# Kernel optimization log

Hardware: AMD Instinct MI355X
Metric: run time of the kernel (lower is better)

The kernel has to match this reference:

```python
import jax, jax.numpy as jnp
import numpy as np

HIDDEN = 1024
HEADS = 16
HEAD_DIM = HIDDEN // HEADS
B, S = 2, 2048


def setup_inputs() -> dict:
    key = jax.random.key(0)
    k1, k2, k3 = jax.random.split(key, 3)
    scale_in = 1.0 / np.sqrt(HIDDEN)
    x = jax.random.normal(k1, (B, S, HIDDEN), dtype=jnp.float32)
    wqkv_w = jax.random.normal(k2, (3 * HIDDEN, HIDDEN), dtype=jnp.float32) * scale_in
    wo_w = jax.random.normal(k3, (HIDDEN, HIDDEN), dtype=jnp.float32) * scale_in
    wo_b = jnp.zeros((HIDDEN,), dtype=jnp.float32)
    return {"x": x, "wqkv_w": wqkv_w, "wo_w": wo_w, "wo_b": wo_b}


def reference(x, wqkv_w, wo_w, wo_b):
    b, s, d = x.shape
    h, hd = HEADS, HEAD_DIM
    sm_scale = hd ** (-0.5)
    # QKV projection (torch Linear: x @ W^T), then chunk into q,k,v
    qkv = jnp.einsum('bsd,ed->bse', x, wqkv_w)  # [b, s, 3d]
    q, k, v = jnp.split(qkv, 3, axis=-1)
    # [b, h, s, hd]
    q = q.reshape(b, s, h, hd).transpose(0, 2, 1, 3)
    k = k.reshape(b, s, h, hd).transpose(0, 2, 1, 3)
    v = v.reshape(b, s, h, hd).transpose(0, 2, 1, 3)
    # raw scores, then causal mask (mask applied BEFORE scaling, as in source;
    # -inf * scale == -inf so math matches softmax(score*scale) with mask)
    scores = jnp.einsum('bhqe,bhke->bhqk', q, k)
    causal = jnp.tril(jnp.ones((s, s), dtype=bool))
    scores = jnp.where(causal[None, None, :, :], scores, -jnp.inf)
    weights = jax.nn.softmax(scores * sm_scale, axis=-1)
    # dropout p=0.0 (eval) -> identity
    out = jnp.einsum('bhqk,bhke->bhqe', weights, v)
    out = out.transpose(0, 2, 1, 3).reshape(b, s, h * hd)
    y = jnp.einsum('bsd,ed->bse', out, wo_w) + wo_b
    return (y, k, v)
```

## Files before the change

kernel.cpp:

```cpp
#include <hip/hip_runtime.h>
#include <cstdint>
#include <cstddef>


using bf16x8 = __attribute__((ext_vector_type(8))) __bf16;
using f32x4  = __attribute__((ext_vector_type(4))) float;
using u16    = unsigned short;

#define SOFT_SCALE 0.1803368801111244f

__device__ __forceinline__ u16 f2bf(float f) {
  union { float f; uint32_t u; } a; a.f = f;
  uint32_t r = a.u + 0x7fffu + ((a.u >> 16) & 1u);
  return (u16)(r >> 16);
}

__device__ __forceinline__ bf16x8 ldfrag(const u16* p) {
  return *reinterpret_cast<const bf16x8*>(p);
}

__device__ __forceinline__ void gload_lds16(const void* g, void* l) {
  __builtin_amdgcn_global_load_lds((const __attribute__((address_space(1))) void*)g,
                                   (__attribute__((address_space(3))) void*)l,
                                   16, 0, 0);
}

__device__ __forceinline__ uint32_t cvt_pk_bf16(float a, float b) {
  uint32_t r;
  asm("v_cvt_pk_bf16_f32 %0, %1, %2" : "=v"(r) : "v"(a), "v"(b));
  return r;
}

__global__ void cvt_all(const float* __restrict__ x, const float* __restrict__ wqkv,
                        const float* __restrict__ wo,
                        u16* __restrict__ xb, u16* __restrict__ wqkvb, u16* __restrict__ wob) {
  int i = blockIdx.x * blockDim.x + threadIdx.x;
  int stride = gridDim.x * blockDim.x;
  for (; i < 2097152; i += stride) {
    const float* src; u16* dst; int j;
    if (i < 1048576)      { src = x;    dst = xb;    j = i; }
    else if (i < 1835008) { src = wqkv; dst = wqkvb; j = i - 1048576; }
    else                  { src = wo;   dst = wob;   j = i - 1835008; }
    float4 v = reinterpret_cast<const float4*>(src)[j];
    ushort4 o;
    o.x = f2bf(v.x); o.y = f2bf(v.y); o.z = f2bf(v.z); o.w = f2bf(v.w);
    reinterpret_cast<ushort4*>(dst)[j] = o;
  }
}

__global__ __launch_bounds__(512, 2) void qkv_gemm_kernel(
    const u16* __restrict__ Xb, const u16* __restrict__ Wb,
    u16* __restrict__ Qws, u16* __restrict__ Kws, u16* __restrict__ Vtws,
    float* __restrict__ out) {
  extern __shared__ char smem[];

  const int tid = threadIdx.x, lane = tid & 63, wid = tid >> 6;
  const int wr = wid >> 2, wc = wid & 3;
  const int fq = lane >> 4, fr = lane & 15;

  const int wg = (blockIdx.x & 7) * 24 + (blockIdx.x >> 3);
  const int bm = wg / 12, bn = wg % 12;
  const int m0 = bm * 256, n0 = bn * 256;

  const char* Ab = (const char*)Xb + (size_t)m0 * 2048;
  const char* Bb = (const char*)Wb + (size_t)n0 * 2048;

  f32x4 acc[8][4] = {};

  auto stage_half = [&](int t, int mat, int h) {
    char* dst = smem + mat * 65536 + (t & 1) * 32768 + h * 16384;
    const char* src = mat ? Bb : Ab;
#pragma unroll
    for (int l = 0; l < 2; ++l) {
      int lin = (l * 512 + tid) * 16;
      int rl  = lin >> 7;
      int col = (lin & 127) ^ ((rl & 7) << 4);
      gload_lds16(src + (size_t)(h * 128 + rl) * 2048 + t * 128 + col, dst + lin);
    }
  };

  stage_half(0, 0, 0); stage_half(0, 0, 1);
  stage_half(0, 1, 0); stage_half(0, 1, 1);
  stage_half(1, 1, 0); stage_half(1, 1, 1);
  asm volatile("s_waitcnt vmcnt(4)" ::: "memory");
  __builtin_amdgcn_s_barrier();

  bf16x8 afr[4][2];
  bf16x8 bfr[4][2];

  for (int t = 0; t < 16; ++t) {
    const char* As = smem + (t & 1) * 32768;
    const char* Bs = smem + 65536 + (t & 1) * 32768;

#pragma unroll
    for (int m = 0; m < 4; ++m) {
      int row = wr * 128 + m * 16 + fr;
#pragma unroll
      for (int ks = 0; ks < 2; ++ks)
        afr[m][ks] = *(const bf16x8*)(As + row * 128 + ((ks * 64 + fq * 16) ^ ((row & 7) << 4)));
    }
#pragma unroll
    for (int n = 0; n < 2; ++n) {
      int row = wc * 64 + n * 16 + fr;
#pragma unroll
      for (int ks = 0; ks < 2; ++ks)
        bfr[n][ks] = *(const bf16x8*)(Bs + row * 128 + ((ks * 64 + fq * 16) ^ ((row & 7) << 4)));
    }
    if (t + 1 < 16) stage_half(t + 1, 0, 0);
    __builtin_amdgcn_s_barrier();
    asm volatile("s_waitcnt lgkmcnt(0)" ::: "memory");
    __builtin_amdgcn_sched_barrier(0);
    __builtin_amdgcn_s_setprio(1);
#pragma unroll
    for (int m = 0; m < 4; ++m)
#pragma unroll
      for (int n = 0; n < 2; ++n)
#pragma unroll
        for (int ks = 0; ks < 2; ++ks)
          acc[m][n] = __builtin_amdgcn_mfma_f32_16x16x32_bf16(afr[m][ks], bfr[n][ks], acc[m][n], 0, 0, 0);
    __builtin_amdgcn_s_setprio(0);
    __builtin_amdgcn_s_barrier();

#pragma unroll
    for (int n = 2; n < 4; ++n) {
      int row = wc * 64 + n * 16 + fr;
#pragma unroll
      for (int ks = 0; ks < 2; ++ks)
        bfr[n][ks] = *(const bf16x8*)(Bs + row * 128 + ((ks * 64 + fq * 16) ^ ((row & 7) << 4)));
    }
    if (t + 1 < 16) stage_half(t + 1, 0, 1);
    __builtin_amdgcn_s_barrier();
    asm volatile("s_waitcnt lgkmcnt(0)" ::: "memory");
    __builtin_amdgcn_sched_barrier(0);
    __builtin_amdgcn_s_setprio(1);
#pragma unroll
    for (int m = 0; m < 4; ++m)
#pragma unroll
      for (int n = 2; n < 4; ++n)
#pragma unroll
        for (int ks = 0; ks < 2; ++ks)
          acc[m][n] = __builtin_amdgcn_mfma_f32_16x16x32_bf16(afr[m][ks], bfr[n][ks], acc[m][n], 0, 0, 0);
    __builtin_amdgcn_s_setprio(0);
    __builtin_amdgcn_s_barrier();

#pragma unroll
    for (int m = 0; m < 4; ++m) {
      int row = wr * 128 + (m + 4) * 16 + fr;
#pragma unroll
      for (int ks = 0; ks < 2; ++ks)
        afr[m][ks] = *(const bf16x8*)(As + row * 128 + ((ks * 64 + fq * 16) ^ ((row & 7) << 4)));
    }
    if (t + 2 < 16) stage_half(t + 2, 1, 0);
    __builtin_amdgcn_s_barrier();
    asm volatile("s_waitcnt lgkmcnt(0)" ::: "memory");
    __builtin_amdgcn_sched_barrier(0);
    __builtin_amdgcn_s_setprio(1);
#pragma unroll
    for (int m = 0; m < 4; ++m)
#pragma unroll
      for (int n = 0; n < 2; ++n)
#pragma unroll
        for (int ks = 0; ks < 2; ++ks)
          acc[m + 4][n] = __builtin_amdgcn_mfma_f32_16x16x32_bf16(afr[m][ks], bfr[n][ks], acc[m + 4][n], 0, 0, 0);
    __builtin_amdgcn_s_setprio(0);
    __builtin_amdgcn_s_barrier();

    if (t + 2 < 16) stage_half(t + 2, 1, 1);
    __builtin_amdgcn_s_barrier();
    __builtin_amdgcn_s_setprio(1);
#pragma unroll
    for (int m = 0; m < 4; ++m)
#pragma unroll
      for (int n = 2; n < 4; ++n)
#pragma unroll
        for (int ks = 0; ks < 2; ++ks)
          acc[m + 4][n] = __builtin_amdgcn_mfma_f32_16x16x32_bf16(afr[m][ks], bfr[n][ks], acc[m + 4][n], 0, 0, 0);
    __builtin_amdgcn_s_setprio(0);
    if (t < 15) {
      if (t == 14) asm volatile("s_waitcnt vmcnt(0)" ::: "memory");
      else         asm volatile("s_waitcnt vmcnt(4)" ::: "memory");
    }
    __builtin_amdgcn_s_barrier();
  }

  const int sect = n0 >> 10;
  const int nn0 = (n0 & 1023) + wc * 64;
  const int mbase = m0 + wr * 128;
#pragma unroll
  for (int m = 0; m < 8; ++m)
#pragma unroll
    for (int n = 0; n < 4; ++n) {
      int mB = mbase + m * 16 + fq * 4;
      int ncol = nn0 + n * 16 + fr;
      int b = mB >> 11, s0 = mB & 2047;
      int h = ncol >> 6, hd = ncol & 63;
      size_t base = (((size_t)b * 16 + h) * 2048 + s0) * 64 + hd;
      float v0 = acc[m][n][0], v1 = acc[m][n][1], v2 = acc[m][n][2], v3 = acc[m][n][3];
      if (sect == 0) {
        Qws[base]       = f2bf(v0 * SOFT_SCALE);
        Qws[base + 64]  = f2bf(v1 * SOFT_SCALE);
        Qws[base + 128] = f2bf(v2 * SOFT_SCALE);
        Qws[base + 192] = f2bf(v3 * SOFT_SCALE);
      } else if (sect == 1) {
        Kws[base] = f2bf(v0); Kws[base + 64] = f2bf(v1);
        Kws[base + 128] = f2bf(v2); Kws[base + 192] = f2bf(v3);
        out[4194304 + base] = v0; out[4194304 + base + 64] = v1;
        out[4194304 + base + 128] = v2; out[4194304 + base + 192] = v3;
      } else {
        out[8388608 + base] = v0; out[8388608 + base + 64] = v1;
        out[8388608 + base + 128] = v2; out[8388608 + base + 192] = v3;
        size_t tt = ((size_t)(b * 16 + h) * 64 + hd) * 2048 + s0;
        ushort4 pk; pk.x = f2bf(v0); pk.y = f2bf(v1); pk.z = f2bf(v2); pk.w = f2bf(v3);
        *reinterpret_cast<ushort4*>(Vtws + tt) = pk;
      }
    }
}

__device__ __forceinline__ void gemm128_core(const u16* __restrict__ A,
                                             const u16* __restrict__ B,
                                             int m0, int n0, int K,
                                             u16* As, u16* Bs, f32x4 acc[4][4]) {
  const int tid  = threadIdx.x;
  const int lane = tid & 63;
  const int wid  = tid >> 6;
  const int wr = wid >> 1, wc = wid & 1;
  const int fq = lane >> 4, fr = lane & 15;

  for (int kb = 0; kb < K; kb += 32) {
#pragma unroll
    for (int j = 0; j < 2; ++j) {
      int lin = (j * 256 + tid) * 16;
      int row = lin >> 6;
      int rb  = lin & 63;
      gload_lds16((const char*)(A + (size_t)(m0 + row) * K + kb) + rb, (char*)As + lin);
      gload_lds16((const char*)(B + (size_t)(n0 + row) * K + kb) + rb, (char*)Bs + lin);
    }
    __syncthreads();

    bf16x8 av[4], bv[4];
#pragma unroll
    for (int i = 0; i < 4; ++i) av[i] = ldfrag(As + (wr * 64 + i * 16 + fr) * 32 + fq * 8);
#pragma unroll
    for (int j = 0; j < 4; ++j) bv[j] = ldfrag(Bs + (wc * 64 + j * 16 + fr) * 32 + fq * 8);
    __builtin_amdgcn_s_setprio(1);
#pragma unroll
    for (int i = 0; i < 4; ++i)
#pragma unroll
      for (int j = 0; j < 4; ++j)
        acc[i][j] = __builtin_amdgcn_mfma_f32_16x16x32_bf16(av[i], bv[j], acc[i][j], 0, 0, 0);
    __builtin_amdgcn_s_setprio(0);
    __syncthreads();
  }
}

__global__ __launch_bounds__(256, 4) void attn_kernel(
    const u16* __restrict__ Qw, const u16* __restrict__ Kw,
    const u16* __restrict__ Vtw, u16* __restrict__ Ow) {
  __shared__ u16 Ks[2][64 * 64];
  __shared__ u16 Vs[2][64 * 64];

  const int tid = threadIdx.x, lane = tid & 63, wid = tid >> 6;
  const int wk = wid >> 1, wh = wid & 1;
  const int fq = lane >> 4, fr = lane & 15;
  const int bh = blockIdx.x & 31;
  const int qb = 31 - (blockIdx.x >> 5);
  const int b = bh >> 4, h = bh & 15;
  const int q0 = qb * 64;

  const u16* Qbase  = Qw  + (size_t)bh * 2048 * 64;
  const u16* Kbase  = Kw  + (size_t)bh * 2048 * 64;
  const char* VtBase = (const char*)(Vtw + (size_t)bh * 64 * 2048);

#pragma unroll
  for (int f = 0; f < 2; ++f) {
    int lin = (f * 256 + tid) * 16;
    int row = lin >> 7;
    int logical = lin ^ ((row & 7) << 4);
    gload_lds16((const char*)Kbase + logical, (char*)Ks[0] + lin);
    gload_lds16(VtBase + (size_t)row * 4096 + (logical & 127), (char*)Vs[0] + lin);
  }

  bf16x8 qa[2][2];
#pragma unroll
  for (int qt = 0; qt < 2; ++qt)
#pragma unroll
    for (int kh = 0; kh < 2; ++kh)
      qa[qt][kh] = ldfrag(Qbase + (size_t)(q0 + wh * 32 + qt * 16 + fr) * 64 + kh * 32 + fq * 8);

  float ssum[2] = {0.f, 0.f};
  f32x4 accO[2][4] = {};

  int cur = 0;
  for (int kb = 0; kb <= qb; ++kb) {
    __syncthreads();

    if (kb < qb) {
      const char* kg = (const char*)(Kbase + (size_t)(kb + 1) * 64 * 64);
#pragma unroll
      for (int f = 0; f < 2; ++f) {
        int lin = (f * 256 + tid) * 16;
        int row = lin >> 7;
        int logical = lin ^ ((row & 7) << 4);
        gload_lds16(kg + logical, (char*)Ks[cur ^ 1] + lin);
        gload_lds16(VtBase + (size_t)row * 4096 + (size_t)(kb + 1) * 128 + (logical & 127),
                    (char*)Vs[cur ^ 1] + lin);
      }
    }

    const u16* Kc = Ks[cur];
    const u16* Vc = Vs[cur];

    f32x4 st[2][2];
    __builtin_amdgcn_s_setprio(1);
#pragma unroll
    for (int kvt = 0; kvt < 2; ++kvt) {
      int krow = wk * 32 + kvt * 16 + fr;
      bf16x8 kf0 = ldfrag(Kc + krow * 64 + ((fq * 8)      ^ ((krow & 7) << 3)));
      bf16x8 kf1 = ldfrag(Kc + krow * 64 + ((fq * 8 + 32) ^ ((krow & 7) << 3)));
#pragma unroll
      for (int qt = 0; qt < 2; ++qt) {
        f32x4 z = {};
        z = __builtin_amdgcn_mfma_f32_16x16x32_bf16(kf0, qa[qt][0], z, 0, 0, 0);
        z = __builtin_amdgcn_mfma_f32_16x16x32_bf16(kf1, qa[qt][1], z, 0, 0, 0);
        st[kvt][qt] = z;
      }
    }
    __builtin_amdgcn_s_setprio(0);

    uint32_t W[2][2][2];
#pragma unroll
    for (int qt = 0; qt < 2; ++qt) {
      int qrow = q0 + wh * 32 + qt * 16 + fr;
#pragma unroll
      for (int kvt = 0; kvt < 2; ++kvt) {
        float p0, p1, p2, p3;
        if (kb < qb) {
          p0 = exp2f(st[kvt][qt][0]);
          p1 = exp2f(st[kvt][qt][1]);
          p2 = exp2f(st[kvt][qt][2]);
          p3 = exp2f(st[kvt][qt][3]);
        } else {
          int kvg = kb * 64 + wk * 32 + kvt * 16 + fq * 4;
          p0 = (kvg + 0 > qrow) ? 0.f : exp2f(st[kvt][qt][0]);
          p1 = (kvg + 1 > qrow) ? 0.f : exp2f(st[kvt][qt][1]);
          p2 = (kvg + 2 > qrow) ? 0.f : exp2f(st[kvt][qt][2]);
          p3 = (kvg + 3 > qrow) ? 0.f : exp2f(st[kvt][qt][3]);
        }
        ssum[qt] += (p0 + p1) + (p2 + p3);
        W[qt][kvt][0] = cvt_pk_bf16(p0, p1);
        W[qt][kvt][1] = cvt_pk_bf16(p2, p3);
      }
    }

    union U { uint32_t u[4]; bf16x8 v; };
    U pa[2];
#pragma unroll
    for (int qt = 0; qt < 2; ++qt)
#pragma unroll
      for (int hh = 0; hh < 2; ++hh) {
        uint32_t a0 = W[qt][0][hh], b0 = W[qt][1][hh];
        asm("v_permlane32_swap_b32 %0, %1" : "+v"(a0), "+v"(b0));
        asm("v_permlane16_swap_b32 %0, %1" : "+v"(a0), "+v"(b0));
        pa[qt].u[hh] = a0; pa[qt].u[2 + hh] = b0;
      }

    __builtin_amdgcn_s_setprio(1);
#pragma unroll
    for (int ht = 0; ht < 4; ++ht) {
      int vrow = ht * 16 + fr;
      bf16x8 vb = ldfrag(Vc + vrow * 64 + ((wk * 32 + fq * 8) ^ ((vrow & 7) << 3)));
#pragma unroll
      for (int qt = 0; qt < 2; ++qt)
        accO[qt][ht] = __builtin_amdgcn_mfma_f32_16x16x32_bf16(pa[qt].v, vb, accO[qt][ht], 0, 0, 0);
    }
    __builtin_amdgcn_s_setprio(0);
    cur ^= 1;
  }

#pragma unroll
  for (int qt = 0; qt < 2; ++qt) {
    ssum[qt] += __shfl_xor(ssum[qt], 16);
    ssum[qt] += __shfl_xor(ssum[qt], 32);
  }

  __syncthreads();
  float* Ored = (float*)Ks;
  float* Sred = (float*)Vs;
  if (wk == 1) {
#pragma unroll
    for (int qt = 0; qt < 2; ++qt)
#pragma unroll
      for (int ht = 0; ht < 4; ++ht)
        *reinterpret_cast<f32x4*>(&Ored[(((wh * 2 + qt) * 4 + ht) << 8) + lane * 4]) = accO[qt][ht];
    if (fq == 0) {
      Sred[wh * 64 + fr]      = ssum[0];
      Sred[wh * 64 + 16 + fr] = ssum[1];
    }
  }
  __syncthreads();
  if (wk == 0) {
#pragma unroll
    for (int qt = 0; qt < 2; ++qt)
#pragma unroll
      for (int ht = 0; ht < 4; ++ht) {
        f32x4 o = *reinterpret_cast<const f32x4*>(&Ored[(((wh * 2 + qt) * 4 + ht) << 8) + lane * 4]);
        accO[qt][ht] += o;
      }
    float invq[2][4];
#pragma unroll
    for (int qt = 0; qt < 2; ++qt) {
      float s = ssum[qt] + Sred[wh * 64 + qt * 16 + fr];
      float inv = 1.0f / s;
#pragma unroll
      for (int r = 0; r < 4; ++r) invq[qt][r] = __shfl(inv, fq * 4 + r);
    }
#pragma unroll
    for (int qt = 0; qt < 2; ++qt)
#pragma unroll
      for (int ht = 0; ht < 4; ++ht)
#pragma unroll
        for (int r = 0; r < 4; ++r) {
          float o = accO[qt][ht][r] * invq[qt][r];
          int qr = q0 + wh * 32 + qt * 16 + fq * 4 + r;
          Ow[((size_t)b * 2048 + qr) * 1024 + h * 64 + ht * 16 + fr] = f2bf(o);
        }
  }
}

__global__ __launch_bounds__(256) void proj_gemm_kernel(
    const u16* __restrict__ Ob, const u16* __restrict__ Wob,
    const float* __restrict__ bias, float* __restrict__ out) {
  __shared__ u16 As[128 * 32];
  __shared__ u16 Bs[128 * 32];
  const int NB = 8;
  int m0 = (blockIdx.x / NB) * 128, n0 = (blockIdx.x % NB) * 128;
  f32x4 acc[4][4] = {};
  gemm128_core(Ob, Wob, m0, n0, 1024, As, Bs, acc);

  const int lane = threadIdx.x & 63, wid = threadIdx.x >> 6;
  const int wr = wid >> 1, wc = wid & 1, fq = lane >> 4, fr = lane & 15;
#pragma unroll
  for (int i = 0; i < 4; ++i)
#pragma unroll
    for (int j = 0; j < 4; ++j)
#pragma unroll
      for (int r = 0; r < 4; ++r) {
        int m = m0 + wr * 64 + i * 16 + fq * 4 + r;
        int n = n0 + wc * 64 + j * 16 + fr;
        out[(size_t)m * 1024 + n] = acc[i][j][r] + bias[n];
      }
}

extern "C" void kernel_launch(void* const* d_in, const int* in_sizes, int n_in,
                              void* d_out, int out_size, void* d_ws, size_t ws_size,
                              hipStream_t stream) {
  const float* x    = (const float*)d_in[0];
  const float* wqkv = (const float*)d_in[1];
  const float* wo   = (const float*)d_in[2];
  const float* wo_b = (const float*)d_in[3];
  float* out = (float*)d_out;

  u16* xb    = (u16*)d_ws;
  u16* wqkvb = xb    + 4194304;
  u16* wob   = wqkvb + 3145728;
  u16* q_ws  = wob   + 1048576;
  u16* k_ws  = q_ws  + 4194304;
  u16* vt_ws = k_ws  + 4194304;
  u16* o_ws  = vt_ws + 4194304;

  static bool attr_set = false;
  if (!attr_set) {
    hipFuncSetAttribute((const void*)qkv_gemm_kernel,
                        hipFuncAttributeMaxDynamicSharedMemorySize, 131072);
    attr_set = true;
  }

  cvt_all<<<2048, 256, 0, stream>>>(x, wqkv, wo, xb, wqkvb, wob);
  qkv_gemm_kernel<<<192, 512, 131072, stream>>>(xb, wqkvb, q_ws, k_ws, vt_ws, out);
  attn_kernel<<<32 * 32, 256, 0, stream>>>(q_ws, k_ws, vt_ws, o_ws);
  proj_gemm_kernel<<<32 * 8, 256, 0, stream>>>(o_ws, wob, wo_b, out);
}
```

Baseline: 116.5 us.

## Retile QKV GEMM to 256x192 tiles so the grid fills all 256 CUs

```diff
diff --git a/kernel.cpp b/kernel.cpp
--- a/kernel.cpp
+++ b/kernel.cpp
@@ -58,39 +58,48 @@
   const int wr = wid >> 2, wc = wid & 3;
   const int fq = lane >> 4, fr = lane & 15;
 
-  const int wg = (blockIdx.x & 7) * 24 + (blockIdx.x >> 3);
-  const int bm = wg / 12, bn = wg % 12;
-  const int m0 = bm * 256, n0 = bn * 256;
+  const int wg = (blockIdx.x & 7) * 32 + (blockIdx.x >> 3);
+  const int bm = wg >> 4, bn = wg & 15;
+  const int m0 = bm * 256, n0 = bn * 192;
 
   const char* Ab = (const char*)Xb + (size_t)m0 * 2048;
   const char* Bb = (const char*)Wb + (size_t)n0 * 2048;
 
-  f32x4 acc[8][4] = {};
-
-  auto stage_half = [&](int t, int mat, int h) {
-    char* dst = smem + mat * 65536 + (t & 1) * 32768 + h * 16384;
-    const char* src = mat ? Bb : Ab;
+  f32x4 acc[8][3] = {};
+
+  auto stage_A = [&](int t, int h) {
+    char* dst = smem + (t & 1) * 32768 + h * 16384;
 #pragma unroll
     for (int l = 0; l < 2; ++l) {
       int lin = (l * 512 + tid) * 16;
       int rl  = lin >> 7;
       int col = (lin & 127) ^ ((rl & 7) << 4);
-      gload_lds16(src + (size_t)(h * 128 + rl) * 2048 + t * 128 + col, dst + lin);
+      gload_lds16(Ab + (size_t)(h * 128 + rl) * 2048 + t * 128 + col, dst + lin);
     }
   };
-
-  stage_half(0, 0, 0); stage_half(0, 0, 1);
-  stage_half(0, 1, 0); stage_half(0, 1, 1);
-  stage_half(1, 1, 0); stage_half(1, 1, 1);
-  asm volatile("s_waitcnt vmcnt(4)" ::: "memory");
+  auto stage_B = [&](int t) {
+    char* dst = smem + 65536 + (t & 1) * 24576;
+#pragma unroll
+    for (int l = 0; l < 3; ++l) {
+      int lin = (l * 512 + tid) * 16;
+      int rl  = lin >> 7;
+      int col = (lin & 127) ^ ((rl & 7) << 4);
+      gload_lds16(Bb + (size_t)rl * 2048 + t * 128 + col, dst + lin);
+    }
+  };
+
+  stage_A(0, 0); stage_A(0, 1);
+  stage_B(0);
+  stage_B(1);
+  asm volatile("s_waitcnt vmcnt(3)" ::: "memory");
   __builtin_amdgcn_s_barrier();
 
   bf16x8 afr[4][2];
-  bf16x8 bfr[4][2];
+  bf16x8 bfr[3][2];
 
   for (int t = 0; t < 16; ++t) {
     const char* As = smem + (t & 1) * 32768;
-    const char* Bs = smem + 65536 + (t & 1) * 32768;
+    const char* Bs = smem + 65536 + (t & 1) * 24576;
 
 #pragma unroll
     for (int m = 0; m < 4; ++m) {
@@ -100,13 +109,13 @@
         afr[m][ks] = *(const bf16x8*)(As + row * 128 + ((ks * 64 + fq * 16) ^ ((row & 7) << 4)));
     }
 #pragma unroll
-    for (int n = 0; n < 2; ++n) {
-      int row = wc * 64 + n * 16 + fr;
+    for (int n = 0; n < 3; ++n) {
+      int row = wc * 48 + n * 16 + fr;
 #pragma unroll
       for (int ks = 0; ks < 2; ++ks)
         bfr[n][ks] = *(const bf16x8*)(Bs + row * 128 + ((ks * 64 + fq * 16) ^ ((row & 7) << 4)));
     }
-    if (t + 1 < 16) stage_half(t + 1, 0, 0);
+    if (t + 1 < 16) stage_A(t + 1, 0);
     __builtin_amdgcn_s_barrier();
     asm volatile("s_waitcnt lgkmcnt(0)" ::: "memory");
     __builtin_amdgcn_sched_barrier(0);
@@ -114,7 +123,7 @@
 #pragma unroll
     for (int m = 0; m < 4; ++m)
 #pragma unroll
-      for (int n = 0; n < 2; ++n)
+      for (int n = 0; n < 3; ++n)
 #pragma unroll
         for (int ks = 0; ks < 2; ++ks)
           acc[m][n] = __builtin_amdgcn_mfma_f32_16x16x32_bf16(afr[m][ks], bfr[n][ks], acc[m][n], 0, 0, 0);
@@ -122,13 +131,14 @@
     __builtin_amdgcn_s_barrier();
 
 #pragma unroll
-    for (int n = 2; n < 4; ++n) {
-      int row = wc * 64 + n * 16 + fr;
+    for (int m = 0; m < 4; ++m) {
+      int row = wr * 128 + (m + 4) * 16 + fr;
 #pragma unroll
       for (int ks = 0; ks < 2; ++ks)
-        bfr[n][ks] = *(const bf16x8*)(Bs + row * 128 + ((ks * 64 + fq * 16) ^ ((row & 7) << 4)));
-    }
-    if (t + 1 < 16) stage_half(t + 1, 0, 1);
+        afr[m][ks] = *(const bf16x8*)(As + row * 128 + ((ks * 64 + fq * 16) ^ ((row & 7) << 4)));
+    }
+    if (t + 1 < 16) stage_A(t + 1, 1);
+    if (t + 2 < 16) stage_B(t + 2);
     __builtin_amdgcn_s_barrier();
     asm volatile("s_waitcnt lgkmcnt(0)" ::: "memory");
     __builtin_amdgcn_sched_barrier(0);
@@ -136,64 +146,27 @@
 #pragma unroll
     for (int m = 0; m < 4; ++m)
 #pragma unroll
-      for (int n = 2; n < 4; ++n)
-#pragma unroll
-        for (int ks = 0; ks < 2; ++ks)
-          acc[m][n] = __builtin_amdgcn_mfma_f32_16x16x32_bf16(afr[m][ks], bfr[n][ks], acc[m][n], 0, 0, 0);
-    __builtin_amdgcn_s_setprio(0);
-    __builtin_amdgcn_s_barrier();
-
-#pragma unroll
-    for (int m = 0; m < 4; ++m) {
-      int row = wr * 128 + (m + 4) * 16 + fr;
-#pragma unroll
-      for (int ks = 0; ks < 2; ++ks)
-        afr[m][ks] = *(const bf16x8*)(As + row * 128 + ((ks * 64 + fq * 16) ^ ((row & 7) << 4)));
-    }
-    if (t + 2 < 16) stage_half(t + 2, 1, 0);
-    __builtin_amdgcn_s_barrier();
-    asm volatile("s_waitcnt lgkmcnt(0)" ::: "memory");
-    __builtin_amdgcn_sched_barrier(0);
-    __builtin_amdgcn_s_setprio(1);
-#pragma unroll
-    for (int m = 0; m < 4; ++m)
-#pragma unroll
-      for (int n = 0; n < 2; ++n)
+      for (int n = 0; n < 3; ++n)
 #pragma unroll
         for (int ks = 0; ks < 2; ++ks)
           acc[m + 4][n] = __builtin_amdgcn_mfma_f32_16x16x32_bf16(afr[m][ks], bfr[n][ks], acc[m + 4][n], 0, 0, 0);
     __builtin_amdgcn_s_setprio(0);
+    if (t < 14)       asm volatile("s_waitcnt vmcnt(3)" ::: "memory");
+    else if (t == 14) asm volatile("s_waitcnt vmcnt(0)" ::: "memory");
     __builtin_amdgcn_s_barrier();
-
-    if (t + 2 < 16) stage_half(t + 2, 1, 1);
-    __builtin_amdgcn_s_barrier();
-    __builtin_amdgcn_s_setprio(1);
-#pragma unroll
-    for (int m = 0; m < 4; ++m)
-#pragma unroll
-      for (int n = 2; n < 4; ++n)
-#pragma unroll
-        for (int ks = 0; ks < 2; ++ks)
-          acc[m + 4][n] = __builtin_amdgcn_mfma_f32_16x16x32_bf16(afr[m][ks], bfr[n][ks], acc[m + 4][n], 0, 0, 0);
-    __builtin_amdgcn_s_setprio(0);
-    if (t < 15) {
-      if (t == 14) asm volatile("s_waitcnt vmcnt(0)" ::: "memory");
-      else         asm volatile("s_waitcnt vmcnt(4)" ::: "memory");
-    }
-    __builtin_amdgcn_s_barrier();
-  }
-
-  const int sect = n0 >> 10;
-  const int nn0 = (n0 & 1023) + wc * 64;
+  }
+
   const int mbase = m0 + wr * 128;
 #pragma unroll
   for (int m = 0; m < 8; ++m)
 #pragma unroll
-    for (int n = 0; n < 4; ++n) {
+    for (int n = 0; n < 3; ++n) {
       int mB = mbase + m * 16 + fq * 4;
-      int ncol = nn0 + n * 16 + fr;
+      int ncol = n0 + wc * 48 + n * 16 + fr;
+      int sect = ncol >> 10;
+      int nn = ncol & 1023;
       int b = mB >> 11, s0 = mB & 2047;
-      int h = ncol >> 6, hd = ncol & 63;
+      int h = nn >> 6, hd = nn & 63;
       size_t base = (((size_t)b * 16 + h) * 2048 + s0) * 64 + hd;
       float v0 = acc[m][n][0], v1 = acc[m][n][1], v2 = acc[m][n][2], v3 = acc[m][n][3];
       if (sect == 0) {
@@ -476,7 +449,7 @@
   }
 
   cvt_all<<<2048, 256, 0, stream>>>(x, wqkv, wo, xb, wqkvb, wob);
-  qkv_gemm_kernel<<<192, 512, 131072, stream>>>(xb, wqkvb, q_ws, k_ws, vt_ws, out);
+  qkv_gemm_kernel<<<256, 512, 114688, stream>>>(xb, wqkvb, q_ws, k_ws, vt_ws, out);
   attn_kernel<<<32 * 32, 256, 0, stream>>>(q_ws, k_ws, vt_ws, o_ws);
   proj_gemm_kernel<<<32 * 8, 256, 0, stream>>>(o_ws, wob, wo_b, out);
 }
```

Measured after the change: 113.8 us. -2.3%, faster.
